# Kernel tuning notes

Measured on AMD Instinct MI355X. Metric: run time of the kernel, lower is better.

The kernel has to match this reference:

```python
import jax, jax.numpy as jnp
import numpy as np

KS = 7           # kernel spatial size (odd)
OMEGA0 = 10.0    # SIREN frequency
PAD = 3          # conv padding ('same' for ks=7)


def _rel_positions_grid(ks):
    # [2, ks, ks], coords in [-1, 1]
    lin = jnp.linspace(-1.0, 1.0, ks, dtype=jnp.float32)
    yy, xx = jnp.meshgrid(lin, lin, indexing='ij')
    return jnp.stack([yy, xx], axis=0)


def _siren(points, W1, b1, W2, b2, W3, b3):
    # points: [..., 3] -> [..., out_ch*in_ch]
    h = jnp.sin(OMEGA0 * (points @ W1 + b1))
    h = jnp.sin(OMEGA0 * (h @ W2 + b2))
    return h @ W3 + b3


def setup_inputs() -> dict:
    key = jax.random.key(0)
    ks = jax.random.split(key, 8)
    B, Cin, Cout, G, H, W, Hid = 16, 32, 32, 8, 64, 64, 32
    x = jax.random.normal(ks[0], (B, Cin, G, H, W), dtype=jnp.float32)
    # deterministic rotation grid on SO(2): angles in [0, 2pi)
    input_g_elems = (jnp.arange(G, dtype=jnp.float32) * (2.0 * jnp.pi / G))[None, :]
    # SIREN params: 3 -> Hid -> Hid -> Cout*Cin
    W1 = jax.random.uniform(ks[1], (3, Hid), minval=-1.0, maxval=1.0) / 3.0
    b1 = jnp.zeros((Hid,), jnp.float32)
    c = jnp.sqrt(6.0 / Hid) / OMEGA0
    W2 = jax.random.uniform(ks[2], (Hid, Hid), minval=-c, maxval=c)
    b2 = jnp.zeros((Hid,), jnp.float32)
    W3 = jax.random.uniform(ks[3], (Hid, Cout * Cin), minval=-c, maxval=c)
    b3 = jnp.zeros((Cout * Cin,), jnp.float32)
    bias = jnp.zeros((1, Cout), jnp.float32)
    return {"x": x, "input_g_elems": input_g_elems, "W1": W1, "b1": b1,
            "W2": W2, "b2": b2, "W3": W3, "b3": b3, "bias": bias}


def reference(x, input_g_elems, W1, b1, W2, b2, W3, b3, bias):
    B, Cin, Gin, H, Wd = x.shape
    Cout = bias.shape[1]
    two_pi = 2.0 * jnp.pi
    rel_pos = _rel_positions_grid(KS)                        # [2, ks, ks]

    # deterministic / non-partial path: g_elems = input_g_elems
    thetas = input_g_elems[0]                                # [G]
    Gout = thetas.shape[0]

    # acted group coords: inv(g) . h = (h - g) mod 2pi, normalized to [-1, 1)
    acted_g = jnp.mod(thetas[None, :] - thetas[:, None], two_pi) / jnp.pi - 1.0  # [Gout, Gin]

    # rotate Rd rel positions by inv(g) = R(-theta)
    ct, st = jnp.cos(-thetas), jnp.sin(-thetas)
    R = jnp.stack([jnp.stack([ct, -st], -1), jnp.stack([st, ct], -1)], -2)  # [Gout,2,2]
    acted_rel = jnp.einsum('gij,jhw->gihw', R, rel_pos)      # [Gout,2,ks,ks]

    # positions fed to kernel net: [Gout, Gin, ks, ks, 3]
    pos_rd = jnp.broadcast_to(acted_rel[:, :, None], (Gout, 2, Gin, KS, KS))
    pos_g = jnp.broadcast_to(acted_g[:, None, :, None, None], (Gout, 1, Gin, KS, KS))
    coords = jnp.concatenate([pos_rd, pos_g], axis=1)        # [Gout,3,Gin,ks,ks]
    points = jnp.moveaxis(coords, 1, -1)                     # [Gout,Gin,ks,ks,3]

    kernel = _siren(points, W1, b1, W2, b2, W3, b3)          # [Gout,Gin,ks,ks,Cout*Cin]
    kernel = kernel.reshape(Gout, Gin, KS, KS, Cout, Cin)
    kernel = jnp.transpose(kernel, (0, 4, 5, 1, 2, 3))       # [Gout,Cout,Cin,Gin,ks,ks]

    # zero kernel outside unit disk of (rotated) Rd positions
    mask = (jnp.linalg.norm(acted_rel, axis=1) <= 1.0)       # [Gout,ks,ks]
    kernel = kernel * mask[:, None, None, None, :, :]

    weight = kernel.reshape(Gout * Cout, Cin * Gin, KS, KS)
    x2 = x.reshape(B, Cin * Gin, H, Wd)
    out = jax.lax.conv_general_dilated(
        x2, weight, window_strides=(1, 1), padding=[(PAD, PAD), (PAD, PAD)],
        dimension_numbers=('NCHW', 'OIHW', 'NCHW'))          # [B, Gout*Cout, H, W]
    out = out.reshape(B, Gout, Cout, H, Wd).transpose(0, 2, 1, 3, 4)  # [B,Cout,Gout,H,W]
    out = out + bias.reshape(1, Cout, 1, 1, 1)
    return out
```

## Files before the change

### kernel.cpp

```cpp
#include <hip/hip_runtime.h>
#include <math.h>

typedef __bf16 bf16_t;
typedef __bf16 bf16x8 __attribute__((ext_vector_type(8)));
typedef float  f32x4  __attribute__((ext_vector_type(4)));

#define B_    16
#define CIN_  32
#define COUT_ 32
#define G_    8
#define CH_   256
#define H_    64
#define W_    64
#define HID_  32
#define KS_   7
#define PAD_  3
#define WP_   70

#define ROW_ELEMS  (WP_ * CH_)
#define XP_ELEMS   ((size_t)B_ * WP_ * ROW_ELEMS)
#define XP_BYTES   (XP_ELEMS * 2)

#define REPACK_BLOCKS (B_ * (H_ + 6))
#define GENW_BLOCKS   (G_ * G_)
#define CONV_BLOCKS   (B_ * (H_ / 2))

static __device__ __forceinline__ unsigned pack_bf16(float a, float b) {
    union { __bf16 h; unsigned short u; } ua, ub;
    ua.h = (__bf16)a; ub.h = (__bf16)b;
    return (unsigned)ua.u | ((unsigned)ub.u << 16);
}

static __device__ __forceinline__ void dma16(const bf16_t* g, bf16_t* l) {
    __builtin_amdgcn_global_load_lds(
        (const __attribute__((address_space(1))) void*)g,
        (__attribute__((address_space(3))) void*)l, 16, 0, 0);
}

__global__ void prep(const float* __restrict__ x, bf16_t* __restrict__ xp,
                     const float* __restrict__ thetas,
                     const float* __restrict__ W1, const float* __restrict__ b1,
                     const float* __restrict__ W2, const float* __restrict__ b2,
                     const float* __restrict__ W3, const float* __restrict__ b3,
                     bf16_t* __restrict__ w2out) {
    __shared__ float h1s[49][33];
    __shared__ float h2s[49][33];
    __shared__ float masks[49];
    int tid = threadIdx.x;
    if (blockIdx.x < REPACK_BLOCKS) {
        int blk = blockIdx.x;
        int b = blk / (H_ + 6), hy = blk % (H_ + 6);
        const int4 z4 = make_int4(0, 0, 0, 0);
        if (hy >= H_) {
            int idx = hy - H_;
            int y = (idx < 3) ? idx : idx + 64;
            bf16_t* dst = xp + ((size_t)(b * WP_) + y) * ROW_ELEMS;
            for (int i = tid; i < ROW_ELEMS / 8; i += 256)
                *reinterpret_cast<int4*>(dst + (size_t)i * 8) = z4;
            return;
        }
        int lane = tid & 63, wv = tid >> 6;
        int r = lane >> 3;
        int t = lane & 7;
        size_t orow = ((size_t)(b * WP_) + (hy + 3)) * ROW_ELEMS;
        for (int it = 0; it < 8; ++it) {
            int c0 = wv * 8 + it * 32;
            const float* src = x + ((size_t)(b * CH_ + c0 + r)) * (H_ * W_)
                                 + (size_t)hy * W_ + t * 8;
            float4 f0 = *reinterpret_cast<const float4*>(src);
            float4 f1 = *reinterpret_cast<const float4*>(src + 4);
            int d0 = (int)pack_bf16(f0.x, f0.y);
            int d1 = (int)pack_bf16(f0.z, f0.w);
            int d2 = (int)pack_bf16(f1.x, f1.y);
            int d3 = (int)pack_bf16(f1.z, f1.w);
            int p0, p1, p2, p3;
            p0 = __shfl_xor(d0, 32); p1 = __shfl_xor(d1, 32);
            p2 = __shfl_xor(d2, 32); p3 = __shfl_xor(d3, 32);
            if ((r & 4) == 0) { d2 = p0; d3 = p1; } else { d0 = p2; d1 = p3; }
            p0 = __shfl_xor(d0, 16); p1 = __shfl_xor(d1, 16);
            p2 = __shfl_xor(d2, 16); p3 = __shfl_xor(d3, 16);
            if ((r & 2) == 0) { d1 = p0; d3 = p2; } else { d0 = p1; d2 = p3; }
            p0 = __shfl_xor(d0, 8); p1 = __shfl_xor(d1, 8);
            p2 = __shfl_xor(d2, 8); p3 = __shfl_xor(d3, 8);
            if ((r & 1) == 0) {
                d0 = (d0 & 0xFFFF) | (p0 << 16);
                d1 = (d1 & 0xFFFF) | (p1 << 16);
                d2 = (d2 & 0xFFFF) | (p2 << 16);
                d3 = (d3 & 0xFFFF) | (p3 << 16);
            } else {
                d0 = (d0 & 0xFFFF0000) | ((unsigned)p0 >> 16);
                d1 = (d1 & 0xFFFF0000) | ((unsigned)p1 >> 16);
                d2 = (d2 & 0xFFFF0000) | ((unsigned)p2 >> 16);
                d3 = (d3 & 0xFFFF0000) | ((unsigned)p3 >> 16);
            }
            int xpos = t * 8 + r + 3;
            int c16 = c0 >> 3;
            int4 v = make_int4(d0, d1, d2, d3);
            *reinterpret_cast<int4*>(xp + orow + ((size_t)c16 * WP_ + xpos) * 8) = v;
        }
        if (tid < 192) {
            int col = tid >> 5, cg = tid & 31;
            int xx = (col < 3) ? col : col + 64;
            *reinterpret_cast<int4*>(xp + orow + ((size_t)cg * WP_ + xx) * 8) = z4;
        }
        return;
    }
    int blk = blockIdx.x - REPACK_BLOCKS;
    int gin = blk & 7, gout = blk >> 3;
    const float TWO_PI = 6.283185307179586f;
    const float PI_F   = 3.14159265358979323846f;
    float th_o = thetas[gout], th_i = thetas[gin];
    float d = fmodf(th_i - th_o, TWO_PI);
    if (d < 0.0f) d += TWO_PI;
    float ag = d / PI_F - 1.0f;
    float ct = cosf(-th_o), st = sinf(-th_o);

    if (tid < 196) {
        int p = tid >> 2, q = tid & 3;
        int ky = p / 7, kx = p % 7;
        float yy = (float)(ky - 3) / 3.0f;
        float xx = (float)(kx - 3) / 3.0f;
        float r0 = ct * yy - st * xx;
        float r1 = st * yy + ct * xx;
        if (q == 0)
            masks[p] = (r0 * r0 + r1 * r1 <= 1.00001f) ? 1.0f : 0.0f;
        #pragma unroll
        for (int jo = 0; jo < 8; ++jo) {
            int j = q * 8 + jo;
            float a = r0 * W1[j] + r1 * W1[32 + j] + ag * W1[64 + j] + b1[j];
            h1s[p][j] = __sinf(10.0f * a);
        }
    }
    __syncthreads();
    if (tid < 196) {
        int p = tid >> 2, q = tid & 3;
        #pragma unroll
        for (int jo = 0; jo < 8; ++jo) {
            int j = q * 8 + jo;
            float a = b2[j];
            #pragma unroll
            for (int i = 0; i < HID_; ++i) a += h1s[p][i] * W2[i * HID_ + j];
            h2s[p][j] = __sinf(10.0f * a);
        }
    }
    __syncthreads();
    for (int rep = 0; rep < 4; ++rep) {
        int o = rep * 256 + tid;
        float w3c[HID_];
        #pragma unroll
        for (int i = 0; i < HID_; ++i) w3c[i] = W3[i * 1024 + o];
        float bb = b3[o];
        int cout = o >> 5, cin = o & 31;
        int k = cin * G_ + gin;
        int n = gout * COUT_ + cout;
        int kc = k >> 5, hi = (k >> 3) & 3, jj = k & 7;
        bf16_t* dst = w2out + (((size_t)kc * 4 + hi) * 256 + n) * 8 + jj;
        for (int p = 0; p < 49; ++p) {
            float a = bb;
            #pragma unroll
            for (int i = 0; i < HID_; ++i) a += h2s[p][i] * w3c[i];
            a *= masks[p];
            dst[(size_t)p * (8 * 4 * 256 * 8)] = (bf16_t)a;
        }
    }
}

#define CONV_STEP(AC, AN, BC, BN, PC, PB, AOF)                                \
  do {                                                                        \
    _Pragma("unroll")                                                         \
    for (int nt = 0; nt < 4; ++nt)                                            \
      BN[nt] = *reinterpret_cast<const bf16x8*>(                              \
          (PB) + wlane_off + (PC) * 8192 + nt * 128);                         \
    _Pragma("unroll")                                                         \
    for (int mt = 0; mt < 4; ++mt) {                                          \
      AN[mt]     = *reinterpret_cast<const bf16x8*>(                          \
          aA + ((PC) * 4 * WP_ + mt * 16) * 8 + (AOF));                       \
      AN[mt + 4] = *reinterpret_cast<const bf16x8*>(                          \
          aB + ((PC) * 4 * WP_ + mt * 16) * 8 + (AOF));                       \
    }                                                                         \
    __builtin_amdgcn_s_setprio(1);                                            \
    _Pragma("unroll")                                                         \
    for (int mt = 0; mt < 8; ++mt)                                            \
      _Pragma("unroll")                                                       \
      for (int nt = 0; nt < 4; ++nt)                                          \
        acc[mt][nt] = __builtin_amdgcn_mfma_f32_16x16x32_bf16(                \
            AC[mt], BC[nt], acc[mt][nt], 0, 0, 0);                            \
    __builtin_amdgcn_s_setprio(0);                                            \
  } while (0)

__launch_bounds__(256, 2)
__global__ void conv_mfma(const bf16_t* __restrict__ xp,
                          const bf16_t* __restrict__ w2,
                          const float* __restrict__ bias,
                          float* __restrict__ out) {
    __shared__ __align__(16) bf16_t lds[2][ROW_ELEMS];
    int blk = blockIdx.x;
    int b = blk >> 5, h0 = (blk & 31) << 1;
    int tid = threadIdx.x;
    int ns = tid >> 6, lane = tid & 63;
    int lm = lane & 15, lq = lane >> 4;
    int wlane_off = lq * 2048 + (ns * 64 + lm) * 8;

    f32x4 acc[8][4];
    #pragma unroll
    for (int i = 0; i < 8; ++i)
        #pragma unroll
        for (int j = 0; j < 4; ++j) {
            f32x4 z = {0.0f, 0.0f, 0.0f, 0.0f};
            acc[i][j] = z;
        }

    const bf16_t* rows = xp + (((size_t)(b * WP_) + h0)) * ROW_ELEMS;
    for (int c = ns; c < 70; c += 4)
        dma16(rows + (size_t)c * 512 + lane * 8, &lds[0][0] + c * 512);

    bf16x8 bcur[4], bnxt[4];
    #pragma unroll
    for (int nt = 0; nt < 4; ++nt)
        bcur[nt] = *reinterpret_cast<const bf16x8*>(w2 + wlane_off + nt * 128);
    __syncthreads();

    for (int ky = 0; ky < KS_; ++ky) {
        const bf16_t* slotA = &lds[ky & 1][0];
        const bf16_t* slotB = &lds[(ky + 1) & 1][0];
        bf16x8 acur[8], anxt[8];
        #pragma unroll
        for (int mt = 0; mt < 4; ++mt) {
            int xr = (lq * WP_ + lm) * 8 + mt * 128;
            acur[mt]     = *reinterpret_cast<const bf16x8*>(&slotA[xr]);
            acur[mt + 4] = *reinterpret_cast<const bf16x8*>(&slotB[xr]);
        }
        #pragma unroll 1
        for (int kx = 0; kx < 7; ++kx) {
            const bf16_t* wkx = w2 + (size_t)(ky * 7 + kx) * 65536;
            const bf16_t* wnx = (ky == 6 && kx == 6) ? wkx : wkx + 65536;
            const bf16_t* aA = slotA + (lq * WP_ + lm + kx) * 8;
            const bf16_t* aB = slotB + (lq * WP_ + lm + kx) * 8;
            CONV_STEP(acur, anxt, bcur, bnxt, 1, wkx, 0);
            CONV_STEP(anxt, acur, bnxt, bcur, 2, wkx, 0);
            CONV_STEP(acur, anxt, bcur, bnxt, 3, wkx, 0);
            CONV_STEP(anxt, acur, bnxt, bcur, 4, wkx, 0);
            CONV_STEP(acur, anxt, bcur, bnxt, 5, wkx, 0);
            CONV_STEP(anxt, acur, bnxt, bcur, 6, wkx, 0);
            CONV_STEP(acur, anxt, bcur, bnxt, 7, wkx, 0);
            CONV_STEP(anxt, acur, bnxt, bcur, 0, wnx, 8);
        }
        if (ky < KS_ - 1) {
            __syncthreads();
            bf16_t* dstslot = &lds[ky & 1][0];
            const bf16_t* src = rows + (size_t)(ky + 2) * ROW_ELEMS;
            for (int c = ns; c < 35; c += 4)
                dma16(src + (size_t)c * 512 + lane * 8, dstslot + c * 512);
            __syncthreads();
        }
    }

    #pragma unroll
    for (int mt = 0; mt < 8; ++mt) {
        int h = h0 + (mt >> 2);
        int wq = (mt & 3) * 16 + lq * 4;
        #pragma unroll
        for (int nt = 0; nt < 4; ++nt) {
            int n = ns * 64 + nt * 16 + lm;
            int gout = n >> 5, cout = n & 31;
            float bv = bias[cout];
            f32x4 v = acc[mt][nt];
            v[0] += bv; v[1] += bv; v[2] += bv; v[3] += bv;
            float* po = out + (((size_t)(b * COUT_ + cout) * G_ + gout) * (H_ * W_)
                               + h * W_ + wq);
            *reinterpret_cast<f32x4*>(po) = v;
        }
    }
}

extern "C" void kernel_launch(void* const* d_in, const int* in_sizes, int n_in,
                              void* d_out, int out_size, void* d_ws, size_t ws_size,
                              hipStream_t stream) {
    const float* x      = (const float*)d_in[0];
    const float* thetas = (const float*)d_in[1];
    const float* W1     = (const float*)d_in[2];
    const float* b1     = (const float*)d_in[3];
    const float* W2     = (const float*)d_in[4];
    const float* b2     = (const float*)d_in[5];
    const float* W3     = (const float*)d_in[6];
    const float* b3     = (const float*)d_in[7];
    const float* bias   = (const float*)d_in[8];
    float* out = (float*)d_out;

    bf16_t* xp = (bf16_t*)d_ws;
    bf16_t* w2 = (bf16_t*)((char*)d_ws + XP_BYTES);

    hipLaunchKernelGGL(prep, dim3(REPACK_BLOCKS + GENW_BLOCKS), dim3(256), 0, stream,
                       x, xp, thetas, W1, b1, W2, b2, W3, b3, w2);
    hipLaunchKernelGGL(conv_mfma, dim3(CONV_BLOCKS), dim3(256), 0, stream,
                       xp, w2, bias, out);
}
```

Measured before the change: 448.0 us.

## Fuse input bf16 repack into conv kernel, staging rows directly from fp32 input

Removes the separate repack pass that wrote a padded channels-last bf16 copy of x to workspace. The conv kernel now loads fp32 input rows, converts and shuffles them into the LDS row buffer itself. This cuts one full write and read of the input through global memory and shrinks the prep launch to weight generation only. In exchange the conv kernel does synchronous register loads and conversion instead of async global-to-LDS DMA, so staging is no longer overlapped, and each input row is re-read and re-converted by several blocks.

Result: slower. 463.6 us (+3.5%).

```diff
diff --git a/kernel.cpp b/kernel.cpp
--- a/kernel.cpp
+++ b/kernel.cpp
@@ -18,10 +18,7 @@
 #define WP_   70
 
 #define ROW_ELEMS  (WP_ * CH_)
-#define XP_ELEMS   ((size_t)B_ * WP_ * ROW_ELEMS)
-#define XP_BYTES   (XP_ELEMS * 2)
-
-#define REPACK_BLOCKS (B_ * (H_ + 6))
+
 #define GENW_BLOCKS   (G_ * G_)
 #define CONV_BLOCKS   (B_ * (H_ / 2))
 
@@ -31,81 +28,16 @@
     return (unsigned)ua.u | ((unsigned)ub.u << 16);
 }
 
-static __device__ __forceinline__ void dma16(const bf16_t* g, bf16_t* l) {
-    __builtin_amdgcn_global_load_lds(
-        (const __attribute__((address_space(1))) void*)g,
-        (__attribute__((address_space(3))) void*)l, 16, 0, 0);
-}
-
-__global__ void prep(const float* __restrict__ x, bf16_t* __restrict__ xp,
-                     const float* __restrict__ thetas,
-                     const float* __restrict__ W1, const float* __restrict__ b1,
-                     const float* __restrict__ W2, const float* __restrict__ b2,
-                     const float* __restrict__ W3, const float* __restrict__ b3,
-                     bf16_t* __restrict__ w2out) {
+__global__ void gen_w(const float* __restrict__ thetas,
+                      const float* __restrict__ W1, const float* __restrict__ b1,
+                      const float* __restrict__ W2, const float* __restrict__ b2,
+                      const float* __restrict__ W3, const float* __restrict__ b3,
+                      bf16_t* __restrict__ w2out) {
     __shared__ float h1s[49][33];
     __shared__ float h2s[49][33];
     __shared__ float masks[49];
     int tid = threadIdx.x;
-    if (blockIdx.x < REPACK_BLOCKS) {
-        int blk = blockIdx.x;
-        int b = blk / (H_ + 6), hy = blk % (H_ + 6);
-        const int4 z4 = make_int4(0, 0, 0, 0);
-        if (hy >= H_) {
-            int idx = hy - H_;
-            int y = (idx < 3) ? idx : idx + 64;
-            bf16_t* dst = xp + ((size_t)(b * WP_) + y) * ROW_ELEMS;
-            for (int i = tid; i < ROW_ELEMS / 8; i += 256)
-                *reinterpret_cast<int4*>(dst + (size_t)i * 8) = z4;
-            return;
-        }
-        int lane = tid & 63, wv = tid >> 6;
-        int r = lane >> 3;
-        int t = lane & 7;
-        size_t orow = ((size_t)(b * WP_) + (hy + 3)) * ROW_ELEMS;
-        for (int it = 0; it < 8; ++it) {
-            int c0 = wv * 8 + it * 32;
-            const float* src = x + ((size_t)(b * CH_ + c0 + r)) * (H_ * W_)
-                                 + (size_t)hy * W_ + t * 8;
-            float4 f0 = *reinterpret_cast<const float4*>(src);
-            float4 f1 = *reinterpret_cast<const float4*>(src + 4);
-            int d0 = (int)pack_bf16(f0.x, f0.y);
-            int d1 = (int)pack_bf16(f0.z, f0.w);
-            int d2 = (int)pack_bf16(f1.x, f1.y);
-            int d3 = (int)pack_bf16(f1.z, f1.w);
-            int p0, p1, p2, p3;
-            p0 = __shfl_xor(d0, 32); p1 = __shfl_xor(d1, 32);
-            p2 = __shfl_xor(d2, 32); p3 = __shfl_xor(d3, 32);
-            if ((r & 4) == 0) { d2 = p0; d3 = p1; } else { d0 = p2; d1 = p3; }
-            p0 = __shfl_xor(d0, 16); p1 = __shfl_xor(d1, 16);
-            p2 = __shfl_xor(d2, 16); p3 = __shfl_xor(d3, 16);
-            if ((r & 2) == 0) { d1 = p0; d3 = p2; } else { d0 = p1; d2 = p3; }
-            p0 = __shfl_xor(d0, 8); p1 = __shfl_xor(d1, 8);
-            p2 = __shfl_xor(d2, 8); p3 = __shfl_xor(d3, 8);
-            if ((r & 1) == 0) {
-                d0 = (d0 & 0xFFFF) | (p0 << 16);
-                d1 = (d1 & 0xFFFF) | (p1 << 16);
-                d2 = (d2 & 0xFFFF) | (p2 << 16);
-                d3 = (d3 & 0xFFFF) | (p3 << 16);
-            } else {
-                d0 = (d0 & 0xFFFF0000) | ((unsigned)p0 >> 16);
-                d1 = (d1 & 0xFFFF0000) | ((unsigned)p1 >> 16);
-                d2 = (d2 & 0xFFFF0000) | ((unsigned)p2 >> 16);
-                d3 = (d3 & 0xFFFF0000) | ((unsigned)p3 >> 16);
-            }
-            int xpos = t * 8 + r + 3;
-            int c16 = c0 >> 3;
-            int4 v = make_int4(d0, d1, d2, d3);
-            *reinterpret_cast<int4*>(xp + orow + ((size_t)c16 * WP_ + xpos) * 8) = v;
-        }
-        if (tid < 192) {
-            int col = tid >> 5, cg = tid & 31;
-            int xx = (col < 3) ? col : col + 64;
-            *reinterpret_cast<int4*>(xp + orow + ((size_t)cg * WP_ + xx) * 8) = z4;
-        }
-        return;
-    }
-    int blk = blockIdx.x - REPACK_BLOCKS;
+    int blk = blockIdx.x;
     int gin = blk & 7, gout = blk >> 3;
     const float TWO_PI = 6.283185307179586f;
     const float PI_F   = 3.14159265358979323846f;
@@ -162,6 +94,61 @@
             a *= masks[p];
             dst[(size_t)p * (8 * 4 * 256 * 8)] = (bf16_t)a;
         }
+    }
+}
+
+static __device__ __forceinline__ void stage_row(bf16_t* slot,
+                                                 const float* __restrict__ x,
+                                                 int b, int ypad, int tid) {
+    const int4 z4 = make_int4(0, 0, 0, 0);
+    if (ypad < 3 || ypad > 66) {
+        for (int i = tid; i < ROW_ELEMS / 8; i += 256)
+            *reinterpret_cast<int4*>(slot + (size_t)i * 8) = z4;
+        return;
+    }
+    int hy = ypad - 3;
+    int lane = tid & 63, wv = tid >> 6;
+    int r = lane >> 3;
+    int t = lane & 7;
+    for (int it = 0; it < 8; ++it) {
+        int c0 = wv * 8 + it * 32;
+        const float* src = x + ((size_t)(b * CH_ + c0 + r)) * (H_ * W_)
+                             + (size_t)hy * W_ + t * 8;
+        float4 f0 = *reinterpret_cast<const float4*>(src);
+        float4 f1 = *reinterpret_cast<const float4*>(src + 4);
+        int d0 = (int)pack_bf16(f0.x, f0.y);
+        int d1 = (int)pack_bf16(f0.z, f0.w);
+        int d2 = (int)pack_bf16(f1.x, f1.y);
+        int d3 = (int)pack_bf16(f1.z, f1.w);
+        int p0, p1, p2, p3;
+        p0 = __shfl_xor(d0, 32); p1 = __shfl_xor(d1, 32);
+        p2 = __shfl_xor(d2, 32); p3 = __shfl_xor(d3, 32);
+        if ((r & 4) == 0) { d2 = p0; d3 = p1; } else { d0 = p2; d1 = p3; }
+        p0 = __shfl_xor(d0, 16); p1 = __shfl_xor(d1, 16);
+        p2 = __shfl_xor(d2, 16); p3 = __shfl_xor(d3, 16);
+        if ((r & 2) == 0) { d1 = p0; d3 = p2; } else { d0 = p1; d2 = p3; }
+        p0 = __shfl_xor(d0, 8); p1 = __shfl_xor(d1, 8);
+        p2 = __shfl_xor(d2, 8); p3 = __shfl_xor(d3, 8);
+        if ((r & 1) == 0) {
+            d0 = (d0 & 0xFFFF) | (p0 << 16);
+            d1 = (d1 & 0xFFFF) | (p1 << 16);
+            d2 = (d2 & 0xFFFF) | (p2 << 16);
+            d3 = (d3 & 0xFFFF) | (p3 << 16);
+        } else {
+            d0 = (d0 & 0xFFFF0000) | ((unsigned)p0 >> 16);
+            d1 = (d1 & 0xFFFF0000) | ((unsigned)p1 >> 16);
+            d2 = (d2 & 0xFFFF0000) | ((unsigned)p2 >> 16);
+            d3 = (d3 & 0xFFFF0000) | ((unsigned)p3 >> 16);
+        }
+        int xpos = t * 8 + r + 3;
+        int c16 = c0 >> 3;
+        *reinterpret_cast<int4*>(slot + ((size_t)c16 * WP_ + xpos) * 8)
+            = make_int4(d0, d1, d2, d3);
+    }
+    if (tid < 192) {
+        int col = tid >> 5, cg = tid & 31;
+        int xx = (col < 3) ? col : col + 64;
+        *reinterpret_cast<int4*>(slot + ((size_t)cg * WP_ + xx) * 8) = z4;
     }
 }
 
@@ -189,7 +176,7 @@
   } while (0)
 
 __launch_bounds__(256, 2)
-__global__ void conv_mfma(const bf16_t* __restrict__ xp,
+__global__ void conv_mfma(const float* __restrict__ x,
                           const bf16_t* __restrict__ w2,
                           const float* __restrict__ bias,
                           float* __restrict__ out) {
@@ -210,9 +197,8 @@
             acc[i][j] = z;
         }
 
-    const bf16_t* rows = xp + (((size_t)(b * WP_) + h0)) * ROW_ELEMS;
-    for (int c = ns; c < 70; c += 4)
-        dma16(rows + (size_t)c * 512 + lane * 8, &lds[0][0] + c * 512);
+    stage_row(&lds[0][0], x, b, h0,     tid);
+    stage_row(&lds[1][0], x, b, h0 + 1, tid);
 
     bf16x8 bcur[4], bnxt[4];
     #pragma unroll
@@ -247,10 +233,7 @@
         }
         if (ky < KS_ - 1) {
             __syncthreads();
-            bf16_t* dstslot = &lds[ky & 1][0];
-            const bf16_t* src = rows + (size_t)(ky + 2) * ROW_ELEMS;
-            for (int c = ns; c < 35; c += 4)
-                dma16(src + (size_t)c * 512 + lane * 8, dstslot + c * 512);
+            stage_row(&lds[ky & 1][0], x, b, h0 + ky + 2, tid);
             __syncthreads();
         }
     }
@@ -287,11 +270,10 @@
     const float* bias   = (const float*)d_in[8];
     float* out = (float*)d_out;
 
-    bf16_t* xp = (bf16_t*)d_ws;
-    bf16_t* w2 = (bf16_t*)((char*)d_ws + XP_BYTES);
-
-    hipLaunchKernelGGL(prep, dim3(REPACK_BLOCKS + GENW_BLOCKS), dim3(256), 0, stream,
-                       x, xp, thetas, W1, b1, W2, b2, W3, b3, w2);
+    bf16_t* w2 = (bf16_t*)d_ws;
+
+    hipLaunchKernelGGL(gen_w, dim3(GENW_BLOCKS), dim3(256), 0, stream,
+                       thetas, W1, b1, W2, b2, W3, b3, w2);
     hipLaunchKernelGGL(conv_mfma, dim3(CONV_BLOCKS), dim3(256), 0, stream,
-                       xp, w2, bias, out);
-}
+                       x, w2, bias, out);
+}
```
